# Performance work log

Measured on AMD Instinct MI355X. Metric: run time of the kernel, lower is better.

The kernel has to match this reference:

```python
import jax, jax.numpy as jnp
import numpy as np

N = 50000          # nodes
E = 1600000        # edges (avg degree 32)
D_MODEL = 128      # input == output dim
HEADS = 4
D_HEAD = D_MODEL // HEADS
N_LAYERS = 3


def _edge_softmax(scores, dst, n):
    # scores: [E, H]; softmax over edges sharing the same destination node
    m = jax.ops.segment_max(scores, dst, num_segments=n)          # [N, H]
    m = jnp.where(jnp.isfinite(m), m, 0.0)                        # empty segments -> -inf guard
    ex = jnp.exp(scores - m[dst])                                 # [E, H]
    denom = jax.ops.segment_sum(ex, dst, num_segments=n)          # [N, H]
    return ex / (denom[dst] + 1e-9)


def _gt_layer(h, src, dst, Wq, Wk, Wv, Wo):
    # h: [N, D]; one multi-head graph-attention (graph transformer) layer
    n = h.shape[0]
    q = (h @ Wq).reshape(n, HEADS, D_HEAD)
    k = (h @ Wk).reshape(n, HEADS, D_HEAD)
    v = (h @ Wv).reshape(n, HEADS, D_HEAD)
    scale = 1.0 / np.sqrt(D_HEAD).astype(np.float32)
    scores = jnp.einsum('ehd,ehd->eh', q[dst], k[src]) * scale    # [E, H]
    alpha = _edge_softmax(scores, dst, n)                         # [E, H]
    agg = jax.ops.segment_sum(alpha[:, :, None] * v[src], dst, num_segments=n)  # [N, H, Dh]
    return agg.reshape(n, D_MODEL) @ Wo


def setup_inputs() -> dict:
    key = jax.random.key(0)
    ks = jax.random.split(key, 16)
    s = 1.0 / np.sqrt(D_MODEL)
    inp = {
        'X':    jax.random.normal(ks[0], (N, 1), jnp.float32),
        'Seed': jax.random.uniform(ks[1], (N, 1), jnp.float32),
        'D':    jax.random.uniform(ks[2], (N, 1), jnp.float32),
        'C':    jax.random.uniform(ks[3], (N, 1), jnp.float32),
        'edge_src': jax.random.randint(ks[4], (E,), 0, N, jnp.int32),
        'edge_dst': jax.random.randint(ks[5], (E,), 0, N, jnp.int32),
        # scalar -> d_model embeddings (Linear(1, d, bias=False))
        'W_seed': jax.random.normal(ks[6], (1, D_MODEL), jnp.float32),
        'W_deg':  jax.random.normal(ks[7], (1, D_MODEL), jnp.float32),
        'W_clu':  jax.random.normal(ks[8], (1, D_MODEL), jnp.float32),
        # 3 graph-transformer layers
        'Wq': jax.random.normal(ks[9],  (N_LAYERS, D_MODEL, D_MODEL), jnp.float32) * s,
        'Wk': jax.random.normal(ks[10], (N_LAYERS, D_MODEL, D_MODEL), jnp.float32) * s,
        'Wv': jax.random.normal(ks[11], (N_LAYERS, D_MODEL, D_MODEL), jnp.float32) * s,
        'Wo': jax.random.normal(ks[12], (N_LAYERS, D_MODEL, D_MODEL), jnp.float32) * s,
        # MLP head: Linear(d,d)+ReLU, Linear(d,1)
        'W1': jax.random.normal(ks[13], (D_MODEL, D_MODEL), jnp.float32) * s,
        'b1': jnp.zeros((D_MODEL,), jnp.float32),
        'W2': jax.random.normal(ks[14], (D_MODEL, 1), jnp.float32) * s,
        'b2': jnp.zeros((1,), jnp.float32),
    }
    return inp


def reference(X, Seed, D, C, edge_src, edge_dst,
              W_seed, W_deg, W_clu, Wq, Wk, Wv, Wo, W1, b1, W2, b2):
    # faithful to original: raw X [N,1] broadcast-added to the embeddings
    h = X + Seed @ W_seed + D @ W_deg + C @ W_clu                 # [N, D_MODEL]
    for i in range(N_LAYERS):
        h = _gt_layer(h, edge_src, edge_dst, Wq[i], Wk[i], Wv[i], Wo[i])
    z = jax.nn.relu(h @ W1 + b1)
    return z @ W2 + b2                                            # [N, 1]
```

## Files before the change

### kernel.cpp

```cpp
#include <hip/hip_runtime.h>
#include <math.h>

#define DM 128
#define WSTRIDE 16384

typedef _Float16 f16x8 __attribute__((ext_vector_type(8)));
typedef _Float16 f16x4 __attribute__((ext_vector_type(4)));
typedef _Float16 f16x2 __attribute__((ext_vector_type(2)));
typedef float f32x4v __attribute__((ext_vector_type(4)));

__device__ __forceinline__ float dpp_xor1_add(float x) {
    int r = __builtin_amdgcn_update_dpp(0, __builtin_bit_cast(int, x), 0xB1, 0xf, 0xf, true);
    return x + __builtin_bit_cast(float, r);
}
__device__ __forceinline__ float dpp_xor2_add(float x) {
    int r = __builtin_amdgcn_update_dpp(0, __builtin_bit_cast(int, x), 0x4E, 0xf, 0xf, true);
    return x + __builtin_bit_cast(float, r);
}
__device__ __forceinline__ uint32_t pkh(float x, float y) {
    f16x2 h = {(_Float16)x, (_Float16)y};
    return __builtin_bit_cast(uint32_t, h);
}

__global__ void count_kernel(const int* __restrict__ edst, int* __restrict__ deg, int E) {
    int e = blockIdx.x * blockDim.x + threadIdx.x;
    if (e < E) atomicAdd(&deg[edst[e]], 1);
}

__global__ void scan1_kernel(const int* __restrict__ in, int* __restrict__ outv,
                             int* __restrict__ bsums, int n) {
    __shared__ int s[256];
    int t = threadIdx.x;
    int i = blockIdx.x * 256 + t;
    int v = (i < n) ? in[i] : 0;
    s[t] = v;
    __syncthreads();
    for (int off = 1; off < 256; off <<= 1) {
        int x = (t >= off) ? s[t - off] : 0;
        __syncthreads();
        s[t] += x;
        __syncthreads();
    }
    if (i < n) outv[i] = s[t];
    if (t == 255) bsums[blockIdx.x] = s[255];
}

__global__ void scan2_kernel(int* __restrict__ bsums, int nb) {
    __shared__ int s[256];
    int t = threadIdx.x;
    int v = (t < nb) ? bsums[t] : 0;
    s[t] = v;
    __syncthreads();
    for (int off = 1; off < 256; off <<= 1) {
        int x = (t >= off) ? s[t - off] : 0;
        __syncthreads();
        s[t] += x;
        __syncthreads();
    }
    if (t < nb) bsums[t] = s[t];
}

__global__ void scan3_kernel(const int* __restrict__ outv, const int* __restrict__ bsums,
                             int* __restrict__ ptr, int* __restrict__ cur, int n) {
    int i = blockIdx.x * 256 + threadIdx.x;
    if (i == 0) ptr[0] = 0;
    if (i < n) {
        int add = (blockIdx.x > 0) ? bsums[blockIdx.x - 1] : 0;
        int incl = outv[i] + add;
        ptr[i + 1] = incl;
        cur[i] = incl - ((i < n) ? (outv[i] - ((i & 255) ? outv[i] - outv[i] : 0)) : 0);
    }
}

__global__ void initcur_kernel(const int* __restrict__ ptr, int* __restrict__ cur, int n) {
    int i = blockIdx.x * blockDim.x + threadIdx.x;
    if (i < n) cur[i] = ptr[i];
}

__global__ void scatter_kernel(const int* __restrict__ esrc, const int* __restrict__ edst,
                               int* __restrict__ cur, int* __restrict__ out, int E) {
    int e = blockIdx.x * blockDim.x + threadIdx.x;
    if (e >= E) return;
    int pos = atomicAdd(&cur[edst[e]], 1);
    out[pos] = esrc[e];
}

__global__ void prepack_kernel(const float* __restrict__ Wq, const float* __restrict__ Wk,
                               const float* __restrict__ Wv, const float* __restrict__ Wo,
                               const float* __restrict__ W1, _Float16* __restrict__ W16) {
    int m = blockIdx.z;
    const float* W;
    if (m < 3)       W = Wq + (size_t)m * DM * DM;
    else if (m < 6)  W = Wk + (size_t)(m - 3) * DM * DM;
    else if (m < 9)  W = Wv + (size_t)(m - 6) * DM * DM;
    else if (m < 12) W = Wo + (size_t)(m - 9) * DM * DM;
    else             W = W1;
    int kb = blockIdx.x, nb = blockIdx.y, l = threadIdx.x;
    int kbase = kb * 32 + (l >> 4) * 8;
    int c = nb * 16 + (l & 15);
    f16x8 v;
#pragma unroll
    for (int j = 0; j < 8; j++) v[j] = (_Float16)W[(kbase + j) * DM + c];
    *reinterpret_cast<f16x8*>(W16 + (size_t)m * WSTRIDE + ((kb * 8 + nb) * 64 + l) * 8) = v;
}

__device__ __forceinline__ void tile_gemm_T(const _Float16* __restrict__ sRow,
                                            const _Float16* __restrict__ W16, int lg, int l,
                                            f32x4v acc[8]) {
#pragma unroll
    for (int nb = 0; nb < 8; nb++) acc[nb] = (f32x4v){0.f, 0.f, 0.f, 0.f};
#pragma unroll
    for (int kb = 0; kb < 4; kb++) {
        f16x8 a = *reinterpret_cast<const f16x8*>(sRow + kb * 32 + lg * 8);
#pragma unroll
        for (int nb = 0; nb < 8; nb++) {
            f16x8 b = *reinterpret_cast<const f16x8*>(&W16[((kb * 8 + nb) * 64 + l) * 8]);
            acc[nb] = __builtin_amdgcn_mfma_f32_16x16x32_f16(b, a, acc[nb], 0, 0, 0);
        }
    }
}

__device__ __forceinline__ f16x4 pk4(const f32x4v a) {
    f16x4 h = {(_Float16)a[0], (_Float16)a[1], (_Float16)a[2], (_Float16)a[3]};
    return h;
}

__device__ __forceinline__ void qkv_store_T(const _Float16* __restrict__ sRow, int lr, int lg,
                                            int l, int rowb, int row0, int n,
                                            const _Float16* __restrict__ Wq16,
                                            const _Float16* __restrict__ Wk16,
                                            const _Float16* __restrict__ Wv16,
                                            _Float16* __restrict__ Qo,
                                            _Float16* __restrict__ KVo) {
    int r = row0 + rowb + lr;
    bool ok = (r < n);
    f32x4v acc[8];
    tile_gemm_T(sRow, Wq16, lg, l, acc);
    if (ok) {
#pragma unroll
        for (int nb = 0; nb < 8; nb++)
            *reinterpret_cast<f16x4*>(Qo + (size_t)r * DM + nb * 16 + lg * 4) = pk4(acc[nb]);
    }
    tile_gemm_T(sRow, Wk16, lg, l, acc);
    if (ok) {
#pragma unroll
        for (int nb = 0; nb < 8; nb++)
            *reinterpret_cast<f16x4*>(KVo + (size_t)r * 256 + nb * 16 + lg * 4) = pk4(acc[nb]);
    }
    tile_gemm_T(sRow, Wv16, lg, l, acc);
    if (ok) {
#pragma unroll
        for (int nb = 0; nb < 8; nb++)
            *reinterpret_cast<f16x4*>(KVo + (size_t)r * 256 + 128 + nb * 16 + lg * 4) =
                pk4(acc[nb]);
    }
}

__global__ __launch_bounds__(256) void fused_embed_qkv_kernel(
    const float* __restrict__ X, const float* __restrict__ Seed,
    const float* __restrict__ Dg, const float* __restrict__ Cl,
    const float* __restrict__ Wseed, const float* __restrict__ Wdeg,
    const float* __restrict__ Wclu,
    const _Float16* __restrict__ Wq16, const _Float16* __restrict__ Wk16,
    const _Float16* __restrict__ Wv16,
    _Float16* __restrict__ Qo, _Float16* __restrict__ KVo, int n) {
    __shared__ _Float16 sH[64 * 136];
    int t = threadIdx.x;
    int row0 = blockIdx.x * 64;
    {
        int row = t >> 2, qt = t & 3;
        int gr = min(row0 + row, n - 1);
        float x = X[gr], sd = Seed[gr], dg = Dg[gr], cl = Cl[gr];
#pragma unroll
        for (int j = 0; j < 8; j++) {
            int c4 = qt * 32 + j * 4;
            float4 ws = *reinterpret_cast<const float4*>(Wseed + c4);
            float4 wd = *reinterpret_cast<const float4*>(Wdeg + c4);
            float4 wc = *reinterpret_cast<const float4*>(Wclu + c4);
            f16x4 h;
            h[0] = (_Float16)(x + sd * ws.x + dg * wd.x + cl * wc.x);
            h[1] = (_Float16)(x + sd * ws.y + dg * wd.y + cl * wc.y);
            h[2] = (_Float16)(x + sd * ws.z + dg * wd.z + cl * wc.z);
            h[3] = (_Float16)(x + sd * ws.w + dg * wd.w + cl * wc.w);
            *reinterpret_cast<f16x4*>(&sH[row * 136 + c4]) = h;
        }
    }
    __syncthreads();
    int w = t >> 6, l = t & 63;
    int lr = l & 15, lg = l >> 4;
    qkv_store_T(sH + (w * 16 + lr) * 136, lr, lg, l, w * 16, row0, n, Wq16, Wk16, Wv16, Qo, KVo);
}

__global__ __launch_bounds__(256) void fused_wo_qkv_kernel(
    const _Float16* __restrict__ Ain, const _Float16* __restrict__ Wo16,
    const _Float16* __restrict__ Wq16, const _Float16* __restrict__ Wk16,
    const _Float16* __restrict__ Wv16,
    _Float16* __restrict__ Qo, _Float16* __restrict__ KVo, int n) {
    __shared__ _Float16 sA[64 * 136];
    __shared__ _Float16 sH[64 * 136];
    int t = threadIdx.x;
    int row0 = blockIdx.x * 64;
#pragma unroll
    for (int p = 0; p < 4; p++) {
        int f = p * 256 + t;
        int r = f >> 4, c8 = (f & 15) * 8;
        int gr = min(row0 + r, n - 1);
        *reinterpret_cast<uint4*>(&sA[r * 136 + c8]) =
            *reinterpret_cast<const uint4*>(Ain + (size_t)gr * DM + c8);
    }
    __syncthreads();
    int w = t >> 6, l = t & 63;
    int lr = l & 15, lg = l >> 4;
    int rowb = w * 16;
    f32x4v acc[8];
    tile_gemm_T(sA + (rowb + lr) * 136, Wo16, lg, l, acc);
#pragma unroll
    for (int nb = 0; nb < 8; nb++)
        *reinterpret_cast<f16x4*>(&sH[(rowb + lr) * 136 + nb * 16 + lg * 4]) = pk4(acc[nb]);
    __syncthreads();
    qkv_store_T(sH + (rowb + lr) * 136, lr, lg, l, rowb, row0, n, Wq16, Wk16, Wv16, Qo, KVo);
}

__global__ __launch_bounds__(256) void fused_wo_mlp_kernel(
    const _Float16* __restrict__ Ain, const _Float16* __restrict__ Wo16,
    const _Float16* __restrict__ W116, const float* __restrict__ b1,
    const float* __restrict__ W2, const float* __restrict__ b2,
    float* __restrict__ out, int n) {
    __shared__ _Float16 sA[64 * 136];
    __shared__ _Float16 sH[64 * 136];
    int t = threadIdx.x;
    int row0 = blockIdx.x * 64;
#pragma unroll
    for (int p = 0; p < 4; p++) {
        int f = p * 256 + t;
        int r = f >> 4, c8 = (f & 15) * 8;
        int gr = min(row0 + r, n - 1);
        *reinterpret_cast<uint4*>(&sA[r * 136 + c8]) =
            *reinterpret_cast<const uint4*>(Ain + (size_t)gr * DM + c8);
    }
    __syncthreads();
    int w = t >> 6, l = t & 63;
    int lr = l & 15, lg = l >> 4;
    int rowb = w * 16;
    f32x4v acc[8];
    tile_gemm_T(sA + (rowb + lr) * 136, Wo16, lg, l, acc);
#pragma unroll
    for (int nb = 0; nb < 8; nb++)
        *reinterpret_cast<f16x4*>(&sH[(rowb + lr) * 136 + nb * 16 + lg * 4]) = pk4(acc[nb]);
    __syncthreads();
    tile_gemm_T(sH + (rowb + lr) * 136, W116, lg, l, acc);
    float part = 0.f;
#pragma unroll
    for (int nb = 0; nb < 8; nb++) {
#pragma unroll
        for (int i = 0; i < 4; i++) {
            int c = nb * 16 + lg * 4 + i;
            part += fmaxf(acc[nb][i] + b1[c], 0.f) * W2[c];
        }
    }
    part += __shfl_xor(part, 16, 64);
    part += __shfl_xor(part, 32, 64);
    int r = row0 + rowb + lr;
    if (lg == 0 && r < n) out[r] = part + b2[0];
}

__global__ __launch_bounds__(256) void attn_kernel(const _Float16* __restrict__ Q,
                                                   const uint32_t* __restrict__ KV,
                                                   const int* __restrict__ ptr,
                                                   const int* __restrict__ esrc,
                                                   _Float16* __restrict__ AGG, int n) {
    int wv = threadIdx.x >> 6;
    int lane = threadIdx.x & 63;
    int node = blockIdx.x * 4 + wv;
    if (node >= n) return;
    int e0 = ptr[node], e1 = ptr[node + 1];
    int q4 = lane >> 4;
    int w = lane & 15;
    _Float16* outbase = AGG + (size_t)node * DM + 8 * w;
    if (e0 >= e1) {
        if (lane < 16) *reinterpret_cast<uint4*>(outbase) = make_uint4(0, 0, 0, 0);
        return;
    }
    const float scale = 0.17677669529663687f * 1.4426950408889634f;
    uint4 qv = *reinterpret_cast<const uint4*>(Q + (size_t)node * DM + 8 * w);
    f16x2 qh0 = __builtin_bit_cast(f16x2, qv.x);
    f16x2 qh1 = __builtin_bit_cast(f16x2, qv.y);
    f16x2 qh2 = __builtin_bit_cast(f16x2, qv.z);
    f16x2 qh3 = __builtin_bit_cast(f16x2, qv.w);

    float m = -1e30f, s = 0.f;
    float a0 = 0.f, a1 = 0.f, a2 = 0.f, a3 = 0.f, a4 = 0.f, a5 = 0.f, a6 = 0.f, a7 = 0.f;

    int last = e1 - 1;
    int S = (e1 - e0 + 3) >> 2;
    int loops = (S + 3) >> 2;

    const uint32_t* kvw = KV + w * 4;

    uint4 k0, v0, k1, v1, k2, v2, k3, v3;
    {
        const uint32_t* r0 = kvw + (size_t)esrc[min(e0 + q4, last)] * 128;
        k0 = *reinterpret_cast<const uint4*>(r0);
        v0 = *reinterpret_cast<const uint4*>(r0 + 64);
        const uint32_t* r1 = kvw + (size_t)esrc[min(e0 + 4 + q4, last)] * 128;
        k1 = *reinterpret_cast<const uint4*>(r1);
        v1 = *reinterpret_cast<const uint4*>(r1 + 64);
        const uint32_t* r2 = kvw + (size_t)esrc[min(e0 + 8 + q4, last)] * 128;
        k2 = *reinterpret_cast<const uint4*>(r2);
        v2 = *reinterpret_cast<const uint4*>(r2 + 64);
        const uint32_t* r3 = kvw + (size_t)esrc[min(e0 + 12 + q4, last)] * 128;
        k3 = *reinterpret_cast<const uint4*>(r3);
        v3 = *reinterpret_cast<const uint4*>(r3 + 64);
    }
    int idxn = esrc[min(e0 + 16 + q4, last)];

#define APROC(kc, vc, bidx)                                                            \
    {                                                                                  \
        float p = __builtin_amdgcn_fdot2(qh0, __builtin_bit_cast(f16x2, (kc).x), 0.f, false); \
        p = __builtin_amdgcn_fdot2(qh1, __builtin_bit_cast(f16x2, (kc).y), p, false);  \
        p = __builtin_amdgcn_fdot2(qh2, __builtin_bit_cast(f16x2, (kc).z), p, false);  \
        p = __builtin_amdgcn_fdot2(qh3, __builtin_bit_cast(f16x2, (kc).w), p, false);  \
        p = dpp_xor1_add(p);                                                           \
        p = dpp_xor2_add(p);                                                           \
        p *= scale;                                                                    \
        p = ((bidx) < e1) ? p : -3.0e38f;                                              \
        float diff = p - m;                                                            \
        if (__any(diff > 8.f)) {                                                       \
            float mn = fmaxf(m, p);                                                    \
            float dd = exp2f(m - mn);                                                  \
            s *= dd;                                                                   \
            a0 *= dd; a1 *= dd; a2 *= dd; a3 *= dd;                                    \
            a4 *= dd; a5 *= dd; a6 *= dd; a7 *= dd;                                    \
            m = mn;                                                                    \
            diff = p - m;                                                              \
        }                                                                              \
        float wg = exp2f(diff);                                                        \
        s += wg;                                                                       \
        f16x2 vh0 = __builtin_bit_cast(f16x2, (vc).x);                                 \
        f16x2 vh1 = __builtin_bit_cast(f16x2, (vc).y);                                 \
        f16x2 vh2 = __builtin_bit_cast(f16x2, (vc).z);                                 \
        f16x2 vh3 = __builtin_bit_cast(f16x2, (vc).w);                                 \
        a0 += wg * (float)vh0[0]; a1 += wg * (float)vh0[1];                            \
        a2 += wg * (float)vh1[0]; a3 += wg * (float)vh1[1];                            \
        a4 += wg * (float)vh2[0]; a5 += wg * (float)vh2[1];                            \
        a6 += wg * (float)vh3[0]; a7 += wg * (float)vh3[1];                            \
    }

#define SUBSTEP(kx, vx)                                                                \
    {                                                                                  \
        uint4 kc = kx, vc = vx;                                                        \
        const uint32_t* r = kvw + (size_t)idxn * 128;                                  \
        kx = *reinterpret_cast<const uint4*>(r);                                       \
        vx = *reinterpret_cast<const uint4*>(r + 64);                                  \
        idxn = esrc[min(b + 20, last)];                                                \
        APROC(kc, vc, b);                                                              \
        b += 4;                                                                        \
    }

    int b = e0 + q4;
    for (int it = 0; it < loops; it++) {
        SUBSTEP(k0, v0);
        SUBSTEP(k1, v1);
        SUBSTEP(k2, v2);
        SUBSTEP(k3, v3);
    }
#undef SUBSTEP
#undef APROC

#pragma unroll
    for (int off = 16; off <= 32; off <<= 1) {
        float m2 = __shfl_xor(m, off, 64);
        float s2 = __shfl_xor(s, off, 64);
        float b0 = __shfl_xor(a0, off, 64), b1 = __shfl_xor(a1, off, 64);
        float b2 = __shfl_xor(a2, off, 64), b3 = __shfl_xor(a3, off, 64);
        float b4 = __shfl_xor(a4, off, 64), b5 = __shfl_xor(a5, off, 64);
        float b6 = __shfl_xor(a6, off, 64), b7 = __shfl_xor(a7, off, 64);
        float mF = fmaxf(m, m2);
        float d1 = exp2f(m - mF), d2 = exp2f(m2 - mF);
        s = s * d1 + s2 * d2;
        a0 = a0 * d1 + b0 * d2; a1 = a1 * d1 + b1 * d2;
        a2 = a2 * d1 + b2 * d2; a3 = a3 * d1 + b3 * d2;
        a4 = a4 * d1 + b4 * d2; a5 = a5 * d1 + b5 * d2;
        a6 = a6 * d1 + b6 * d2; a7 = a7 * d1 + b7 * d2;
        m = mF;
    }

    float inv = 1.f / (s + 1e-9f);
    if (lane < 16) {
        uint4 o;
        o.x = pkh(a0 * inv, a1 * inv);
        o.y = pkh(a2 * inv, a3 * inv);
        o.z = pkh(a4 * inv, a5 * inv);
        o.w = pkh(a6 * inv, a7 * inv);
        *reinterpret_cast<uint4*>(outbase) = o;
    }
}

extern "C" void kernel_launch(void* const* d_in, const int* in_sizes, int n_in,
                              void* d_out, int out_size, void* d_ws, size_t ws_size,
                              hipStream_t stream) {
    const float* X    = (const float*)d_in[0];
    const float* Seed = (const float*)d_in[1];
    const float* Dg   = (const float*)d_in[2];
    const float* Cl   = (const float*)d_in[3];
    const int* esrc   = (const int*)d_in[4];
    const int* edst   = (const int*)d_in[5];
    const float* Wseed = (const float*)d_in[6];
    const float* Wdeg  = (const float*)d_in[7];
    const float* Wclu  = (const float*)d_in[8];
    const float* Wq = (const float*)d_in[9];
    const float* Wk = (const float*)d_in[10];
    const float* Wv = (const float*)d_in[11];
    const float* Wo = (const float*)d_in[12];
    const float* W1 = (const float*)d_in[13];
    const float* b1 = (const float*)d_in[14];
    const float* W2 = (const float*)d_in[15];
    const float* b2 = (const float*)d_in[16];
    float* out = (float*)d_out;

    int n = in_sizes[0];
    int E = in_sizes[4];

    char* p = (char*)d_ws;
    auto alloc = [&](size_t bytes) {
        void* r = (void*)p;
        p += (bytes + 255) & ~(size_t)255;
        return r;
    };
    _Float16* qbuf = (_Float16*)alloc((size_t)n * DM * 2);
    _Float16* abuf = (_Float16*)alloc((size_t)n * DM * 2);
    unsigned short* kvbuf = (unsigned short*)alloc((size_t)n * 256 * 2);
    _Float16* W16 = (_Float16*)alloc((size_t)13 * WSTRIDE * 2);
    int* deg    = (int*)alloc((size_t)n * 4);
    int* ptr    = (int*)alloc((size_t)(n + 1) * 4);
    int* ptrtmp = (int*)alloc((size_t)n * 4);
    int* bsums  = (int*)alloc(1024);
    int* cur    = (int*)alloc((size_t)n * 4);
    int* esrcs  = (int*)alloc((size_t)E * 4);
    (void)ws_size; (void)n_in; (void)out_size;

    hipMemsetAsync(deg, 0, (size_t)n * 4, stream);

    int nb = (n + 255) / 256;
    count_kernel<<<(E + 255) / 256, 256, 0, stream>>>(edst, deg, E);
    scan1_kernel<<<nb, 256, 0, stream>>>(deg, ptrtmp, bsums, n);
    scan2_kernel<<<1, 256, 0, stream>>>(bsums, nb);
    scan3_kernel<<<nb, 256, 0, stream>>>(ptrtmp, bsums, ptr, cur, n);
    initcur_kernel<<<nb, 256, 0, stream>>>(ptr, cur, n);
    scatter_kernel<<<(E + 255) / 256, 256, 0, stream>>>(esrc, edst, cur, esrcs, E);

    prepack_kernel<<<dim3(4, 8, 13), 64, 0, stream>>>(Wq, Wk, Wv, Wo, W1, W16);

    int ggrid = (n + 63) / 64;
    int agrid = (n + 3) / 4;
    const uint32_t* KVc = (const uint32_t*)kvbuf;

    fused_embed_qkv_kernel<<<ggrid, 256, 0, stream>>>(
        X, Seed, Dg, Cl, Wseed, Wdeg, Wclu,
        W16 + (size_t)0 * WSTRIDE, W16 + (size_t)3 * WSTRIDE, W16 + (size_t)6 * WSTRIDE,
        qbuf, (_Float16*)kvbuf, n);
    attn_kernel<<<agrid, 256, 0, stream>>>(qbuf, KVc, ptr, esrcs, abuf, n);
    for (int i = 0; i < 2; i++) {
        fused_wo_qkv_kernel<<<ggrid, 256, 0, stream>>>(
            abuf, W16 + (size_t)(9 + i) * WSTRIDE,
            W16 + (size_t)(1 + i) * WSTRIDE, W16 + (size_t)(4 + i) * WSTRIDE,
            W16 + (size_t)(7 + i) * WSTRIDE, qbuf, (_Float16*)kvbuf, n);
        attn_kernel<<<agrid, 256, 0, stream>>>(qbuf, KVc, ptr, esrcs, abuf, n);
    }
    fused_wo_mlp_kernel<<<ggrid, 256, 0, stream>>>(
        abuf, W16 + (size_t)11 * WSTRIDE, W16 + (size_t)12 * WSTRIDE, b1, W2, b2, out, n);
}
```

Measured before the change: 722.1 us.

## Build CSR via two-level bucket partition instead of global scatter

Replaces the single global atomic scatter of edge sources into CSR order with a two-pass scheme. Edges are first partitioned into 256-node destination buckets, using a block-local histogram and bucket atomics. Per-bucket blocks then scatter within a localized range, so the per-node cursor atomics and writes hit a small region. It also drops the initcur kernel by computing cursors in scan3. The cost is an extra 8-byte-per-edge pairs buffer with a full write and read, one more kernel launch, and heavily contended bucket atomics.

```diff
diff --git a/kernel.cpp b/kernel.cpp
--- a/kernel.cpp
+++ b/kernel.cpp
@@ -22,17 +22,28 @@
     return __builtin_bit_cast(uint32_t, h);
 }
 
-__global__ void count_kernel(const int* __restrict__ edst, int* __restrict__ deg, int E) {
-    int e = blockIdx.x * blockDim.x + threadIdx.x;
-    if (e < E) atomicAdd(&deg[edst[e]], 1);
-}
-
-__global__ void scan1_kernel(const int* __restrict__ in, int* __restrict__ outv,
-                             int* __restrict__ bsums, int n) {
+
+__global__ void hist_kernel(const int* __restrict__ edst, int* __restrict__ deg,
+                            int* __restrict__ bcount, int E) {
+    __shared__ int lh[256];
+    int t = threadIdx.x;
+    lh[t] = 0;
+    __syncthreads();
+    int e = blockIdx.x * 256 + t;
+    if (e < E) {
+        int d = edst[e];
+        atomicAdd(&deg[d], 1);
+        atomicAdd(&lh[d >> 8], 1);
+    }
+    __syncthreads();
+    if (lh[t] > 0) atomicAdd(&bcount[t], lh[t]);
+}
+
+__global__ void bscan_kernel(const int* __restrict__ bcount, int* __restrict__ bptr,
+                             int* __restrict__ bcur, int NB) {
     __shared__ int s[256];
     int t = threadIdx.x;
-    int i = blockIdx.x * 256 + t;
-    int v = (i < n) ? in[i] : 0;
+    int v = (t < NB) ? bcount[t] : 0;
     s[t] = v;
     __syncthreads();
     for (int off = 1; off < 256; off <<= 1) {
@@ -41,14 +52,19 @@
         s[t] += x;
         __syncthreads();
     }
-    if (i < n) outv[i] = s[t];
-    if (t == 255) bsums[blockIdx.x] = s[255];
-}
-
-__global__ void scan2_kernel(int* __restrict__ bsums, int nb) {
+    if (t == 0) bptr[0] = 0;
+    if (t < NB) {
+        bptr[t + 1] = s[t];
+        bcur[t] = s[t] - v;
+    }
+}
+
+__global__ void scan1_kernel(const int* __restrict__ in, int* __restrict__ outv,
+                             int* __restrict__ bsums, int n) {
     __shared__ int s[256];
     int t = threadIdx.x;
-    int v = (t < nb) ? bsums[t] : 0;
+    int i = blockIdx.x * 256 + t;
+    int v = (i < n) ? in[i] : 0;
     s[t] = v;
     __syncthreads();
     for (int off = 1; off < 256; off <<= 1) {
@@ -57,32 +73,56 @@
         s[t] += x;
         __syncthreads();
     }
+    if (i < n) outv[i] = s[t];
+    if (t == 255) bsums[blockIdx.x] = s[255];
+}
+
+__global__ void scan2_kernel(int* __restrict__ bsums, int nb) {
+    __shared__ int s[256];
+    int t = threadIdx.x;
+    int v = (t < nb) ? bsums[t] : 0;
+    s[t] = v;
+    __syncthreads();
+    for (int off = 1; off < 256; off <<= 1) {
+        int x = (t >= off) ? s[t - off] : 0;
+        __syncthreads();
+        s[t] += x;
+        __syncthreads();
+    }
     if (t < nb) bsums[t] = s[t];
 }
 
 __global__ void scan3_kernel(const int* __restrict__ outv, const int* __restrict__ bsums,
-                             int* __restrict__ ptr, int* __restrict__ cur, int n) {
+                             const int* __restrict__ deg, int* __restrict__ ptr,
+                             int* __restrict__ cur, int n) {
     int i = blockIdx.x * 256 + threadIdx.x;
     if (i == 0) ptr[0] = 0;
     if (i < n) {
         int add = (blockIdx.x > 0) ? bsums[blockIdx.x - 1] : 0;
         int incl = outv[i] + add;
         ptr[i + 1] = incl;
-        cur[i] = incl - ((i < n) ? (outv[i] - ((i & 255) ? outv[i] - outv[i] : 0)) : 0);
-    }
-}
-
-__global__ void initcur_kernel(const int* __restrict__ ptr, int* __restrict__ cur, int n) {
-    int i = blockIdx.x * blockDim.x + threadIdx.x;
-    if (i < n) cur[i] = ptr[i];
-}
-
-__global__ void scatter_kernel(const int* __restrict__ esrc, const int* __restrict__ edst,
-                               int* __restrict__ cur, int* __restrict__ out, int E) {
+        cur[i] = incl - deg[i];
+    }
+}
+
+__global__ void partition_kernel(const int* __restrict__ esrc, const int* __restrict__ edst,
+                                 int* __restrict__ bcur, int2* __restrict__ pairs, int E) {
     int e = blockIdx.x * blockDim.x + threadIdx.x;
     if (e >= E) return;
-    int pos = atomicAdd(&cur[edst[e]], 1);
-    out[pos] = esrc[e];
+    int d = edst[e];
+    int pos = atomicAdd(&bcur[d >> 8], 1);
+    pairs[pos] = make_int2(esrc[e], d);
+}
+
+__global__ void scatter2_kernel(const int2* __restrict__ pairs, const int* __restrict__ bptr,
+                                int* __restrict__ cur, int* __restrict__ out) {
+    int b = blockIdx.x;
+    int start = bptr[b], end = bptr[b + 1];
+    for (int i = start + threadIdx.x; i < end; i += blockDim.x) {
+        int2 pr = pairs[i];
+        int pos = atomicAdd(&cur[pr.y], 1);
+        out[pos] = pr.x;
+    }
 }
 
 __global__ void prepack_kernel(const float* __restrict__ Wq, const float* __restrict__ Wk,
@@ -420,6 +460,7 @@
 
     int n = in_sizes[0];
     int E = in_sizes[4];
+    int NB = (n + 255) >> 8;
 
     char* p = (char*)d_ws;
     auto alloc = [&](size_t bytes) {
@@ -436,18 +477,25 @@
     int* ptrtmp = (int*)alloc((size_t)n * 4);
     int* bsums  = (int*)alloc(1024);
     int* cur    = (int*)alloc((size_t)n * 4);
+    int* bcount = (int*)alloc(1024);
+    int* bptr   = (int*)alloc(1040);
+    int* bcur   = (int*)alloc(1024);
+    int2* pairs = (int2*)alloc((size_t)E * 8);
     int* esrcs  = (int*)alloc((size_t)E * 4);
     (void)ws_size; (void)n_in; (void)out_size;
 
     hipMemsetAsync(deg, 0, (size_t)n * 4, stream);
+    hipMemsetAsync(bcount, 0, 1024, stream);
 
     int nb = (n + 255) / 256;
-    count_kernel<<<(E + 255) / 256, 256, 0, stream>>>(edst, deg, E);
+    int eb = (E + 255) / 256;
+    hist_kernel<<<eb, 256, 0, stream>>>(edst, deg, bcount, E);
+    bscan_kernel<<<1, 256, 0, stream>>>(bcount, bptr, bcur, NB);
     scan1_kernel<<<nb, 256, 0, stream>>>(deg, ptrtmp, bsums, n);
     scan2_kernel<<<1, 256, 0, stream>>>(bsums, nb);
-    scan3_kernel<<<nb, 256, 0, stream>>>(ptrtmp, bsums, ptr, cur, n);
-    initcur_kernel<<<nb, 256, 0, stream>>>(ptr, cur, n);
-    scatter_kernel<<<(E + 255) / 256, 256, 0, stream>>>(esrc, edst, cur, esrcs, E);
+    scan3_kernel<<<nb, 256, 0, stream>>>(ptrtmp, bsums, deg, ptr, cur, n);
+    partition_kernel<<<eb, 256, 0, stream>>>(esrc, edst, bcur, pairs, E);
+    scatter2_kernel<<<NB, 256, 0, stream>>>(pairs, bptr, cur, esrcs);
 
     prepack_kernel<<<dim3(4, 8, 13), 64, 0, stream>>>(Wq, Wk, Wv, Wo, W1, W16);
 
```

After: 1.636 ms. +126.5%, slower.
